# Kernel optimization log

Hardware: AMD Instinct MI355X
Metric: run time of the kernel (lower is better)

The kernel has to match this reference:

```python
import jax, jax.numpy as jnp
from jax import lax
import numpy as np

C_IN, C_OUT = 8, 16
H_IN = W_IN = 56
S = 28  # input_size: side of the original network input (symbolic coeff map)
K = 3
STRIDE = (1, 1)
PAD = ((1, 1), (1, 1))
DIL = (1, 1)


def setup_inputs() -> dict:
    key = jax.random.key(0)
    k = jax.random.split(key, 6)
    return {
        "lx_in": jax.random.normal(k[0], (C_IN, H_IN, W_IN, S, S), jnp.float32),
        "ux_in": jax.random.normal(k[1], (C_IN, H_IN, W_IN, S, S), jnp.float32),
        "lc_in": jax.random.normal(k[2], (C_IN, H_IN, W_IN), jnp.float32),
        "uc_in": jax.random.normal(k[3], (C_IN, H_IN, W_IN), jnp.float32),
        "weight": jax.random.normal(k[4], (C_OUT, C_IN, K, K), jnp.float32),
        "bias": jax.random.normal(k[5], (C_OUT,), jnp.float32),
    }


def _conv_sym(x, w):
    # x: (Cin, H, W, S, S) symbolic coefficient maps -> fold (S,S) into conv batch
    Cin, Hh, Ww, S1, S2 = x.shape
    xb = x.reshape(Cin, Hh, Ww, S1 * S2).transpose(3, 0, 1, 2)  # (S*S, Cin, H, W)
    y = lax.conv_general_dilated(xb, w, STRIDE, PAD, rhs_dilation=DIL)
    _, Cout, Ho, Wo = y.shape
    return y.transpose(1, 2, 3, 0).reshape(Cout, Ho, Wo, S1, S2)


def _conv_const(c, w):
    # c: (Cin, H, W) constant offsets -> batch of 1
    y = lax.conv_general_dilated(c[None], w, STRIDE, PAD, rhs_dilation=DIL)
    return y[0]  # (Cout, Ho, Wo)


def reference(lx_in, ux_in, lc_in, uc_in, weight, bias):
    # sign-split weights: strictly positive / strictly negative parts (zeros drop out)
    w_pos = jnp.where(weight > 0, weight, 0.0)
    w_neg = jnp.where(weight < 0, weight, 0.0)
    # Interval-bound conv: lower bound mixes lower coeffs through w_pos and
    # upper coeffs through w_neg (and symmetrically for the upper bound).
    lx_out = _conv_sym(lx_in, w_pos) + _conv_sym(ux_in, w_neg)
    ux_out = _conv_sym(ux_in, w_pos) + _conv_sym(lx_in, w_neg)
    lc_out = _conv_const(lc_in, w_pos) + _conv_const(uc_in, w_neg) + bias[:, None, None]
    uc_out = _conv_const(uc_in, w_pos) + _conv_const(lc_in, w_neg) + bias[:, None, None]
    return (lx_out, ux_out, lc_out, uc_out)
```

## Files before the change

### kernel.cpp

```cpp
#include <hip/hip_runtime.h>

#define CIN   8
#define COUT  16
#define HH    56
#define WW    56
#define SS    784
#define PLANE (HH * WW * SS)
#define ROW   (WW * SS)
#define NF2   (HH * WW * (SS / 2))
#define SYM_OUT_SZ (COUT * PLANE)

typedef float f32x2 __attribute__((ext_vector_type(2)));

#if defined(__has_builtin)
#if __has_builtin(__builtin_elementwise_fma)
#define PK_FMA(a, b, c) __builtin_elementwise_fma((a), (b), (c))
#endif
#endif
#ifndef PK_FMA
#define PK_FMA(a, b, c) ((a) * (b) + (c))
#endif

__global__ __launch_bounds__(256) void ibp_prep_w(
    const float* __restrict__ wgt, float* __restrict__ wtr)
{
    const int i = blockIdx.x * 256 + threadIdx.x;
    if (i >= 72 * 16) return;
    const int tap = i >> 4, co = i & 15;
    const int ci = tap / 9, r = tap - ci * 9;
    const float w = wgt[(co * CIN + ci) * 9 + r];
    wtr[tap * 32 + co]      = 0.5f * w;
    wtr[tap * 32 + 16 + co] = 0.5f * fabsf(w);
}

__global__ __launch_bounds__(256) void ibp_conv_sym(
    const float* __restrict__ lx, const float* __restrict__ ux,
    const float* __restrict__ wtr,
    float* __restrict__ lx_out, float* __restrict__ ux_out)
{
    const int tid = threadIdx.x;
    const int b   = blockIdx.x;
    const int vblk = (b < 4800) ? ((b & 7) * 600 + (b >> 3)) : b;
    const int gv   = vblk * 256 + tid;

    const int j2   = gv % 392;
    const int t    = gv / 392;
    const int wi   = t & 7;
    const int hb   = t >> 3;
    const int h    = hb % 56;
    const int band = hb / 56;
    const int w    = band * 8 + wi;

    const int pix  = h * WW + w;
    const int base = pix * SS + j2 * 2;

    const float* bl0 = lx + base;
    const float* bu0 = ux + base;

    f32x2 A[COUT], B[COUT];
    #pragma unroll
    for (int co = 0; co < COUT; ++co) {
        A[co] = (f32x2)0.f;
        B[co] = (f32x2)0.f;
    }

    for (int ci = 0; ci < CIN; ++ci) {
        const float* bl = bl0 + ci * PLANE;
        const float* bu = bu0 + ci * PLANE;
        #pragma unroll
        for (int dh = 0; dh < 3; ++dh) {
            const int ih = h + dh - 1;
            const bool vh = (unsigned)ih < (unsigned)HH;
            #pragma unroll
            for (int dw = 0; dw < 3; ++dw) {
                const int iw = w + dw - 1;
                const bool ok = vh && ((unsigned)iw < (unsigned)WW);
                const int off = (dh - 1) * ROW + (dw - 1) * SS;
                f32x2 lv = (f32x2)0.f, uv = (f32x2)0.f;
                if (ok) {
                    lv = *(const f32x2*)(bl + off);
                    uv = *(const f32x2*)(bu + off);
                }
                const f32x2 s = lv + uv;
                const f32x2 d = lv - uv;

                const int tap = ci * 9 + dh * 3 + dw;
                const float* wp = wtr + tap * 32;
                #pragma unroll
                for (int co = 0; co < COUT; ++co) {
                    const float wa = wp[co];
                    const float wb = wp[16 + co];
                    const f32x2 wa2 = {wa, wa};
                    const f32x2 wb2 = {wb, wb};
                    A[co] = PK_FMA(wa2, s, A[co]);
                    B[co] = PK_FMA(wb2, d, B[co]);
                }
            }
        }
    }

    #pragma unroll
    for (int co = 0; co < COUT; ++co) {
        const f32x2 lo = A[co] + B[co];
        const f32x2 uo = A[co] - B[co];
        __builtin_nontemporal_store(lo, (f32x2*)(lx_out + (size_t)co * PLANE + base));
        __builtin_nontemporal_store(uo, (f32x2*)(ux_out + (size_t)co * PLANE + base));
    }
}

__global__ __launch_bounds__(256) void ibp_conv_const(
    const float* __restrict__ lc, const float* __restrict__ uc,
    const float* __restrict__ wgt, const float* __restrict__ bias,
    float* __restrict__ lc_out, float* __restrict__ uc_out)
{
    const int idx = blockIdx.x * 256 + threadIdx.x;
    if (idx >= COUT * HH * WW) return;
    const int co  = idx / (HH * WW);
    const int pix = idx - co * (HH * WW);
    const int h = pix / WW, w = pix - (pix / WW) * WW;

    float Aa = 0.f, Bb = 0.f;
    for (int ci = 0; ci < CIN; ++ci) {
        #pragma unroll
        for (int dh = 0; dh < 3; ++dh) {
            const int ih = h + dh - 1;
            if ((unsigned)ih >= (unsigned)HH) continue;
            #pragma unroll
            for (int dw = 0; dw < 3; ++dw) {
                const int iw = w + dw - 1;
                if ((unsigned)iw >= (unsigned)WW) continue;
                const float l = lc[(ci * HH + ih) * WW + iw];
                const float u = uc[(ci * HH + ih) * WW + iw];
                const float wv = wgt[((co * CIN + ci) * 3 + dh) * 3 + dw];
                Aa += wv * (l + u);
                Bb += fabsf(wv) * (l - u);
            }
        }
    }
    const float b = bias[co];
    lc_out[idx] = 0.5f * (Aa + Bb) + b;
    uc_out[idx] = 0.5f * (Aa - Bb) + b;
}

extern "C" void kernel_launch(void* const* d_in, const int* in_sizes, int n_in,
                              void* d_out, int out_size, void* d_ws, size_t ws_size,
                              hipStream_t stream) {
    const float* lx   = (const float*)d_in[0];
    const float* ux   = (const float*)d_in[1];
    const float* lc   = (const float*)d_in[2];
    const float* uc   = (const float*)d_in[3];
    const float* wgt  = (const float*)d_in[4];
    const float* bias = (const float*)d_in[5];

    float* out    = (float*)d_out;
    float* lx_out = out;
    float* ux_out = out + (size_t)SYM_OUT_SZ;
    float* lc_out = out + (size_t)2 * SYM_OUT_SZ;
    float* uc_out = lc_out + COUT * HH * WW;

    float* wtr = (float*)d_ws;

    ibp_prep_w<<<(72 * 16 + 255) / 256, 256, 0, stream>>>(wgt, wtr);

    ibp_conv_sym<<<NF2 / 256, 256, 0, stream>>>(lx, ux, wtr, lx_out, ux_out);

    const int nconst = COUT * HH * WW;
    ibp_conv_const<<<(nconst + 255) / 256, 256, 0, stream>>>(
        lc, uc, wgt, bias, lc_out, uc_out);
}
```

Measured before the change: 647.5 us.

## Compute two adjacent output columns per thread to reuse input loads

Each thread now computes two horizontally adjacent output pixels, loading a 4-wide column window per row so that each loaded input pair is shared across both outputs. This cuts global load instructions per output from 9 to 6 per input channel and amortizes the weight loads. The cost is doubling the accumulator register count (64 packed accumulators), which may lower occupancy. The grid is halved and the block remapping is adjusted to match.

```diff
diff --git a/kernel.cpp b/kernel.cpp
--- a/kernel.cpp
+++ b/kernel.cpp
@@ -7,8 +7,10 @@
 #define SS    784
 #define PLANE (HH * WW * SS)
 #define ROW   (WW * SS)
-#define NF2   (HH * WW * (SS / 2))
 #define SYM_OUT_SZ (COUT * PLANE)
+#define NJ2   (SS / 2)
+#define NPAIR (HH * (WW / 2))
+#define NTHREADS (NPAIR * NJ2)
 
 typedef float f32x2 __attribute__((ext_vector_type(2)));
 
@@ -38,73 +40,93 @@
     const float* __restrict__ wtr,
     float* __restrict__ lx_out, float* __restrict__ ux_out)
 {
-    const int tid = threadIdx.x;
-    const int b   = blockIdx.x;
-    const int vblk = (b < 4800) ? ((b & 7) * 600 + (b >> 3)) : b;
-    const int gv   = vblk * 256 + tid;
+    const int t = threadIdx.x;
+    const int b = blockIdx.x;
+    const int vblk = (b < 2400) ? ((b & 7) * 300 + (b >> 3)) : b;
+    const int gv   = vblk * 256 + t;
 
-    const int j2   = gv % 392;
-    const int t    = gv / 392;
-    const int wi   = t & 7;
-    const int hb   = t >> 3;
-    const int h    = hb % 56;
-    const int band = hb / 56;
-    const int w    = band * 8 + wi;
+    const int j2 = gv % NJ2;
+    const int pp = gv / NJ2;
+    const int h  = pp / (WW / 2);
+    const int wp = pp - h * (WW / 2);
+    const int w0 = wp * 2;
+    const int j  = j2 * 2;
 
-    const int pix  = h * WW + w;
-    const int base = pix * SS + j2 * 2;
+    int cok[4];
+    int coff[4];
+    #pragma unroll
+    for (int c = 0; c < 4; ++c) {
+        const int wc = w0 - 1 + c;
+        cok[c]  = (unsigned)wc < (unsigned)WW;
+        coff[c] = cok[c] ? (wc * SS + j) : 0;
+    }
 
-    const float* bl0 = lx + base;
-    const float* bu0 = ux + base;
-
-    f32x2 A[COUT], B[COUT];
+    f32x2 A0[COUT], B0[COUT], A1[COUT], B1[COUT];
     #pragma unroll
     for (int co = 0; co < COUT; ++co) {
-        A[co] = (f32x2)0.f;
-        B[co] = (f32x2)0.f;
+        A0[co] = (f32x2)0.f; B0[co] = (f32x2)0.f;
+        A1[co] = (f32x2)0.f; B1[co] = (f32x2)0.f;
     }
 
     for (int ci = 0; ci < CIN; ++ci) {
-        const float* bl = bl0 + ci * PLANE;
-        const float* bu = bu0 + ci * PLANE;
+        const float* lp = lx + (size_t)ci * PLANE;
+        const float* up = ux + (size_t)ci * PLANE;
+        const float* wci = wtr + ci * 9 * 32;
         #pragma unroll
         for (int dh = 0; dh < 3; ++dh) {
             const int ih = h + dh - 1;
-            const bool vh = (unsigned)ih < (unsigned)HH;
+            const bool rv = (unsigned)ih < (unsigned)HH;
+            const int rbase = ih * ROW;
+
+            f32x2 s[4], d[4];
             #pragma unroll
-            for (int dw = 0; dw < 3; ++dw) {
-                const int iw = w + dw - 1;
-                const bool ok = vh && ((unsigned)iw < (unsigned)WW);
-                const int off = (dh - 1) * ROW + (dw - 1) * SS;
+            for (int c = 0; c < 4; ++c) {
                 f32x2 lv = (f32x2)0.f, uv = (f32x2)0.f;
-                if (ok) {
-                    lv = *(const f32x2*)(bl + off);
-                    uv = *(const f32x2*)(bu + off);
+                if (rv && cok[c]) {
+                    lv = *(const f32x2*)(lp + rbase + coff[c]);
+                    uv = *(const f32x2*)(up + rbase + coff[c]);
                 }
-                const f32x2 s = lv + uv;
-                const f32x2 d = lv - uv;
+                s[c] = lv + uv;
+                d[c] = lv - uv;
+            }
 
-                const int tap = ci * 9 + dh * 3 + dw;
-                const float* wp = wtr + tap * 32;
-                #pragma unroll
-                for (int co = 0; co < COUT; ++co) {
-                    const float wa = wp[co];
-                    const float wb = wp[16 + co];
-                    const f32x2 wa2 = {wa, wa};
-                    const f32x2 wb2 = {wb, wb};
-                    A[co] = PK_FMA(wa2, s, A[co]);
-                    B[co] = PK_FMA(wb2, d, B[co]);
-                }
+            const float* wt = wci + dh * 3 * 32;
+            #pragma unroll
+            for (int co = 0; co < COUT; ++co) {
+                const float wa0 = wt[co],       wb0 = wt[16 + co];
+                const float wa1 = wt[32 + co],  wb1 = wt[48 + co];
+                const float wa2 = wt[64 + co],  wb2 = wt[80 + co];
+                const f32x2 a0 = {wa0, wa0}, a1 = {wa1, wa1}, a2 = {wa2, wa2};
+                const f32x2 b0 = {wb0, wb0}, b1 = {wb1, wb1}, b2 = {wb2, wb2};
+                A0[co] = PK_FMA(a0, s[0], A0[co]);
+                A0[co] = PK_FMA(a1, s[1], A0[co]);
+                A0[co] = PK_FMA(a2, s[2], A0[co]);
+                B0[co] = PK_FMA(b0, d[0], B0[co]);
+                B0[co] = PK_FMA(b1, d[1], B0[co]);
+                B0[co] = PK_FMA(b2, d[2], B0[co]);
+                A1[co] = PK_FMA(a0, s[1], A1[co]);
+                A1[co] = PK_FMA(a1, s[2], A1[co]);
+                A1[co] = PK_FMA(a2, s[3], A1[co]);
+                B1[co] = PK_FMA(b0, d[1], B1[co]);
+                B1[co] = PK_FMA(b1, d[2], B1[co]);
+                B1[co] = PK_FMA(b2, d[3], B1[co]);
             }
         }
     }
 
+    const size_t fb0 = (size_t)(h * WW + w0) * SS + j;
+    const size_t fb1 = fb0 + SS;
     #pragma unroll
     for (int co = 0; co < COUT; ++co) {
-        const f32x2 lo = A[co] + B[co];
-        const f32x2 uo = A[co] - B[co];
-        __builtin_nontemporal_store(lo, (f32x2*)(lx_out + (size_t)co * PLANE + base));
-        __builtin_nontemporal_store(uo, (f32x2*)(ux_out + (size_t)co * PLANE + base));
+        const size_t cb = (size_t)co * PLANE;
+        const f32x2 lo0 = A0[co] + B0[co];
+        const f32x2 uo0 = A0[co] - B0[co];
+        const f32x2 lo1 = A1[co] + B1[co];
+        const f32x2 uo1 = A1[co] - B1[co];
+        __builtin_nontemporal_store(lo0, (f32x2*)(lx_out + cb + fb0));
+        __builtin_nontemporal_store(uo0, (f32x2*)(ux_out + cb + fb0));
+        __builtin_nontemporal_store(lo1, (f32x2*)(lx_out + cb + fb1));
+        __builtin_nontemporal_store(uo1, (f32x2*)(ux_out + cb + fb1));
     }
 }
 
@@ -162,7 +184,7 @@
 
     ibp_prep_w<<<(72 * 16 + 255) / 256, 256, 0, stream>>>(wgt, wtr);
 
-    ibp_conv_sym<<<NF2 / 256, 256, 0, stream>>>(lx, ux, wtr, lx_out, ux_out);
+    ibp_conv_sym<<<NTHREADS / 256, 256, 0, stream>>>(lx, ux, wtr, lx_out, ux_out);
 
     const int nconst = COUT * HH * WW;
     ibp_conv_const<<<(nconst + 255) / 256, 256, 0, stream>>>(
```

New measurement: 563.2 us. -13.0%, faster.
